# Kernel optimization log

Measured on AMD Instinct MI355X. Metric: run time of the kernel, lower is better.

Reference implementation:

```python
import jax, jax.numpy as jnp
import numpy as np

R_PARAM = 3.9
EPS = 0.3
BETA = 0.15
STEPS = 15
CLAMP_LO = 1e-4
CLAMP_HI = 1.0 - 1e-4


def _depthwise_conv3x3(x, k):
    # x: [B, C, H, W], k: [C, 1, 3, 3] (OIHW with feature_group_count=C)
    C = x.shape[1]
    return jax.lax.conv_general_dilated(
        x, k, window_strides=(1, 1), padding=((1, 1), (1, 1)),
        dimension_numbers=("NCHW", "OIHW", "NCHW"), feature_group_count=C)


def setup_inputs() -> dict:
    key = jax.random.key(0)
    k1, k2 = jax.random.split(key)
    drive = jax.random.uniform(k1, (16, 8, 256, 256), dtype=jnp.float32)
    K_raw = jnp.abs(jax.random.uniform(k2, (8, 1, 3, 3), dtype=jnp.float32))
    K_local = K_raw / K_raw.sum(axis=(-1, -2), keepdims=True)  # per-channel sum-to-1
    return {"drive": drive, "K_local": K_local}


def reference(drive, K_local):
    def step(grid, _):
        mapped = R_PARAM * grid * (1.0 - grid)
        local = _depthwise_conv3x3(mapped, K_local)
        physics = (1.0 - EPS) * mapped + EPS * local
        g = (1.0 - BETA) * physics + BETA * drive
        g = jnp.clip(g, CLAMP_LO, CLAMP_HI)
        return g, g

    last, states = jax.lax.scan(step, drive, None, length=STEPS)
    mean = states.mean(axis=0)
    var = ((states - mean) ** 2).mean(axis=0)  # unbiased=False
    delta = last - drive       # first == drive
    last_drive = last - drive
    return (last, mean, var, delta, last_drive)
```

## Files before the change

### kernel.cpp

```cpp
#include <hip/hip_runtime.h>
#include <cstddef>

namespace {

constexpr int IMG = 256;
constexpr long long N_ELEM = 16LL * 8 * IMG * IMG;

constexpr int NTHR   = 1024;
constexpr int DSTR   = 256;
constexpr int DSLOTS = 32;
constexpr int DBUF   = DSLOTS * DSTR;

constexpr float RP   = 3.9f;
constexpr float BET  = 0.15f;
constexpr float IBET = 1.0f / 0.15f;
constexpr float KF   = 0.255f;
constexpr float CF   = 0.595f;
constexpr float CLO  = 1e-4f;
constexpr float CHI  = (float)(1.0 - 1e-4);

__device__ __forceinline__ float mapf(float g) {
    float t = RP * g;
    return fmaf(-t, g, t);
}

__device__ __forceinline__ float dpp_up(float x) {
    return __int_as_float(__builtin_amdgcn_update_dpp(
        0, __float_as_int(x), 0x138, 0xf, 0xf, true));
}
__device__ __forceinline__ float dpp_dn(float x) {
    return __int_as_float(__builtin_amdgcn_update_dpp(
        0, __float_as_int(x), 0x130, 0xf, 0xf, true));
}

__device__ __forceinline__ float px9(const float k2[9],
        float a0, float a1, float a2, float b0, float b1, float b2,
        float c0, float c1, float c2, float bdv) {
    float a = bdv;
    a = fmaf(k2[0], a0, a); a = fmaf(k2[1], a1, a); a = fmaf(k2[2], a2, a);
    a = fmaf(k2[3], b0, a); a = fmaf(k2[4], b1, a); a = fmaf(k2[5], b2, a);
    a = fmaf(k2[6], c0, a); a = fmaf(k2[7], c1, a); a = fmaf(k2[8], c2, a);
    a = fmaf(CF, b1, a);
    return __builtin_amdgcn_fmed3f(a, CLO, CHI);
}

#define WINQ(W, QX, QY, QZ, QW) {                       \
    W[1] = (QX); W[2] = (QY); W[3] = (QZ); W[4] = (QW); \
    W[0] = dpp_up(QW);                                  \
    W[5] = dpp_dn(QX);                                  \
}

#define ROWB(WA, WB, WC, BDV, SUM, SQ, STG, OWN, F) {                                      \
    float g0 = px9(k2, WA[0],WA[1],WA[2], WB[0],WB[1],WB[2], WC[0],WC[1],WC[2], BDV.x);    \
    float g1 = px9(k2, WA[1],WA[2],WA[3], WB[1],WB[2],WB[3], WC[1],WC[2],WC[3], BDV.y);    \
    float g2 = px9(k2, WA[2],WA[3],WA[4], WB[2],WB[3],WB[4], WC[2],WC[3],WC[4], BDV.z);    \
    float g3 = px9(k2, WA[3],WA[4],WA[5], WB[3],WB[4],WB[5], WC[3],WC[4],WC[5], BDV.w);    \
    if (OWN) {                                                                             \
        SUM.x += g0; SUM.y += g1; SUM.z += g2; SUM.w += g3;                                \
        SQ.x = fmaf(g0,g0,SQ.x); SQ.y = fmaf(g1,g1,SQ.y);                                  \
        SQ.z = fmaf(g2,g2,SQ.z); SQ.w = fmaf(g3,g3,SQ.w);                                  \
    }                                                                                      \
    if (F) { STG.x = g0; STG.y = g1; STG.z = g2; STG.w = g3; }                             \
    else   { STG.x = mapf(g0); STG.y = mapf(g1); STG.z = mapf(g2); STG.w = mapf(g3); }     \
}

#define QLOAD(DR) \
    float4 qL, qR;                                                              \
    if (wv > 0)  qL = *(const float4*)((DR) + (2*wv - 1) * DSTR + c4);          \
    else { qL.x = 0.f; qL.y = 0.f; qL.z = 0.f; qL.w = 0.f; }                    \
    if (wv < 15) qR = *(const float4*)((DR) + (2*wv + 2) * DSTR + c4);          \
    else { qR.x = 0.f; qR.y = 0.f; qR.z = 0.f; qR.w = 0.f; }

#define STEP6(F, DR, DW) {                                                      \
    QLOAD(DR)                                                                   \
    float wA[6], wB[6], wC[6];                                                  \
    WINQ(wA, qL.x, qL.y, qL.z, qL.w)                                            \
    WINQ(wB, stg0.x, stg0.y, stg0.z, stg0.w)                                    \
    WINQ(wC, stg1.x, stg1.y, stg1.z, stg1.w)                                    \
    ROWB(wA, wB, wC, bdv0, sum0, sq0, stg0, ow0, F)                             \
    WINQ(wA, stg2.x, stg2.y, stg2.z, stg2.w)                                    \
    ROWB(wB, wC, wA, bdv1, sum1, sq1, stg1, ow1, F)                             \
    WINQ(wB, stg3.x, stg3.y, stg3.z, stg3.w)                                    \
    ROWB(wC, wA, wB, bdv2, sum2, sq2, stg2, ow2, F)                             \
    WINQ(wC, stg4.x, stg4.y, stg4.z, stg4.w)                                    \
    ROWB(wA, wB, wC, bdv3, sum3, sq3, stg3, ow3, F)                             \
    WINQ(wA, stg5.x, stg5.y, stg5.z, stg5.w)                                    \
    ROWB(wB, wC, wA, bdv4, sum4, sq4, stg4, ow4, F)                             \
    WINQ(wB, qR.x, qR.y, qR.z, qR.w)                                            \
    ROWB(wC, wA, wB, bdv5, sum5, sq5, stg5, ow5, F)                             \
    if (!(F)) {                                                                 \
        *(float4*)((DW) + (2*wv    ) * DSTR + c4) = stg0;                       \
        *(float4*)((DW) + (2*wv + 1) * DSTR + c4) = stg5;                       \
    }                                                                           \
}

#define STEP5(F, DR, DW) {                                                      \
    QLOAD(DR)                                                                   \
    float wA[6], wB[6], wC[6];                                                  \
    WINQ(wA, qL.x, qL.y, qL.z, qL.w)                                            \
    WINQ(wB, stg0.x, stg0.y, stg0.z, stg0.w)                                    \
    WINQ(wC, stg1.x, stg1.y, stg1.z, stg1.w)                                    \
    ROWB(wA, wB, wC, bdv0, sum0, sq0, stg0, ow0, F)                             \
    WINQ(wA, stg2.x, stg2.y, stg2.z, stg2.w)                                    \
    ROWB(wB, wC, wA, bdv1, sum1, sq1, stg1, ow1, F)                             \
    WINQ(wB, stg3.x, stg3.y, stg3.z, stg3.w)                                    \
    ROWB(wC, wA, wB, bdv2, sum2, sq2, stg2, ow2, F)                             \
    WINQ(wC, stg4.x, stg4.y, stg4.z, stg4.w)                                    \
    ROWB(wA, wB, wC, bdv3, sum3, sq3, stg3, ow3, F)                             \
    WINQ(wA, qR.x, qR.y, qR.z, qR.w)                                            \
    ROWB(wB, wC, wA, bdv4, sum4, sq4, stg4, ow4, F)                             \
    if (!(F)) {                                                                 \
        *(float4*)((DW) + (2*wv    ) * DSTR + c4) = stg0;                       \
        *(float4*)((DW) + (2*wv + 1) * DSTR + c4) = stg4;                       \
    }                                                                           \
}

#define INITROW(I, STRIDE) {                                                     \
    const int y = y0 + STRIDE * wv + (I);                                        \
    float4 t = *(const float4*)(dimg + y * IMG + c4);                            \
    stg##I.x = mapf(t.x); stg##I.y = mapf(t.y);                                  \
    stg##I.z = mapf(t.z); stg##I.w = mapf(t.w);                                  \
    bdv##I.x = BET * t.x; bdv##I.y = BET * t.y;                                  \
    bdv##I.z = BET * t.z; bdv##I.w = BET * t.w;                                  \
    sum##I.x = 0.f; sum##I.y = 0.f; sum##I.z = 0.f; sum##I.w = 0.f;              \
    sq##I = sum##I; }

#define EPISTORE(I) {                                                             \
    size_t base = (size_t)img * (IMG*IMG) + (size_t)y * IMG + c4;                 \
    float mn0 = sum##I.x*inv15, mn1 = sum##I.y*inv15;                             \
    float mn2 = sum##I.z*inv15, mn3 = sum##I.w*inv15;                             \
    float4 m4; m4.x=mn0; m4.y=mn1; m4.z=mn2; m4.w=mn3;                            \
    float4 v4;                                                                    \
    v4.x = fmaxf(fmaf(-mn0, mn0, sq##I.x*inv15), 0.f);                            \
    v4.y = fmaxf(fmaf(-mn1, mn1, sq##I.y*inv15), 0.f);                            \
    v4.z = fmaxf(fmaf(-mn2, mn2, sq##I.z*inv15), 0.f);                            \
    v4.w = fmaxf(fmaf(-mn3, mn3, sq##I.w*inv15), 0.f);                            \
    float4 d4;                                                                    \
    d4.x = fmaf(-bdv##I.x, IBET, stg##I.x); d4.y = fmaf(-bdv##I.y, IBET, stg##I.y);\
    d4.z = fmaf(-bdv##I.z, IBET, stg##I.z); d4.w = fmaf(-bdv##I.w, IBET, stg##I.w);\
    *(float4*)(out + 0*N_ELEM + base) = stg##I;                                   \
    *(float4*)(out + 1*N_ELEM + base) = m4;                                       \
    *(float4*)(out + 2*N_ELEM + base) = v4;                                       \
    *(float4*)(out + 3*N_ELEM + base) = d4;                                       \
    *(float4*)(out + 4*N_ELEM + base) = d4; }

__device__ __forceinline__ void run_int(const float* __restrict__ drive,
                                        const float* __restrict__ Kl,
                                        float* __restrict__ out,
                                        int img, int ty, float* __restrict__ lds)
{
    float* Da = lds;
    float* Db = lds + DBUF;
    const int tid  = threadIdx.x;
    const int lane = tid & 63;
    const int wv   = tid >> 6;
    const int c4   = lane * 4;

    const int lt = 6 * wv + 4;
    const int lb = 6 * (15 - wv) + 4;
    const int lim = min(15, min(lt, lb));

    const bool ow0 = (6*wv+0 >= 16) && (6*wv+0 <= 79);
    const bool ow1 = (6*wv+1 >= 16) && (6*wv+1 <= 79);
    const bool ow2 = (6*wv+2 >= 16) && (6*wv+2 <= 79);
    const bool ow3 = (6*wv+3 >= 16) && (6*wv+3 <= 79);
    const bool ow4 = (6*wv+4 >= 16) && (6*wv+4 <= 79);
    const bool ow5 = (6*wv+5 >= 16) && (6*wv+5 <= 79);

    const int ch = img & 7;
    float k2[9];
#pragma unroll
    for (int i = 0; i < 9; ++i) k2[i] = KF * Kl[ch * 9 + i];

    const float* dimg = drive + (size_t)img * (IMG * IMG);
    const int y0 = ty * 64 - 16;

    float4 bdv0,bdv1,bdv2,bdv3,bdv4,bdv5;
    float4 stg0,stg1,stg2,stg3,stg4,stg5;
    float4 sum0,sum1,sum2,sum3,sum4,sum5;
    float4 sq0,sq1,sq2,sq3,sq4,sq5;

    INITROW(0,6) INITROW(1,6) INITROW(2,6) INITROW(3,6) INITROW(4,6) INITROW(5,6)

    *(float4*)(Da + (2*wv    ) * DSTR + c4) = stg0;
    *(float4*)(Da + (2*wv + 1) * DSTR + c4) = stg5;
    __syncthreads();

#pragma unroll 1
    for (int s2 = 0; s2 < 7; ++s2) {
        if (2 * s2 < lim)     { STEP6(0, Da, Db) }
        __syncthreads();
        if (2 * s2 + 1 < lim) { STEP6(0, Db, Da) }
        __syncthreads();
    }
    if (lim >= 15) { STEP6(1, Da, Db) }

    if (wv >= 2 && wv <= 13) {
        const float inv15 = 1.0f / 15.0f;
#define EPI6(I) { const int r = 6*wv + (I);                                       \
        if (r >= 16 && r <= 79) { const int y = y0 + r; EPISTORE(I) } }
        EPI6(0) EPI6(1) EPI6(2) EPI6(3) EPI6(4) EPI6(5)
#undef EPI6
    }
}

template<bool TOP>
__device__ __forceinline__ void run_edge(const float* __restrict__ drive,
                                         const float* __restrict__ Kl,
                                         float* __restrict__ out,
                                         int img, float* __restrict__ lds)
{
    float* Da = lds;
    float* Db = lds + DBUF;
    const int tid  = threadIdx.x;
    const int lane = tid & 63;
    const int wv   = tid >> 6;
    const int c4   = lane * 4;

    const int lim = TOP ? min(15, 78 - 5 * wv) : min(15, 3 + 5 * wv);

    const bool ow0 = TOP ? (5*wv+0 <= 63) : (5*wv+0 >= 16);
    const bool ow1 = TOP ? (5*wv+1 <= 63) : (5*wv+1 >= 16);
    const bool ow2 = TOP ? (5*wv+2 <= 63) : (5*wv+2 >= 16);
    const bool ow3 = TOP ? (5*wv+3 <= 63) : (5*wv+3 >= 16);
    const bool ow4 = TOP ? (5*wv+4 <= 63) : (5*wv+4 >= 16);

    const int ch = img & 7;
    float k2[9];
#pragma unroll
    for (int i = 0; i < 9; ++i) k2[i] = KF * Kl[ch * 9 + i];

    const float* dimg = drive + (size_t)img * (IMG * IMG);
    const int y0 = TOP ? 0 : 176;

    float4 bdv0,bdv1,bdv2,bdv3,bdv4;
    float4 stg0,stg1,stg2,stg3,stg4;
    float4 sum0,sum1,sum2,sum3,sum4;
    float4 sq0,sq1,sq2,sq3,sq4;

    INITROW(0,5) INITROW(1,5) INITROW(2,5) INITROW(3,5) INITROW(4,5)

    *(float4*)(Da + (2*wv    ) * DSTR + c4) = stg0;
    *(float4*)(Da + (2*wv + 1) * DSTR + c4) = stg4;
    __syncthreads();

#pragma unroll 1
    for (int s2 = 0; s2 < 7; ++s2) {
        if (2 * s2 < lim)     { STEP5(0, Da, Db) }
        __syncthreads();
        if (2 * s2 + 1 < lim) { STEP5(0, Db, Da) }
        __syncthreads();
    }
    if (lim >= 15) { STEP5(1, Da, Db) }

    const bool own = TOP ? (wv <= 12) : (wv >= 3);
    if (own) {
        const float inv15 = 1.0f / 15.0f;
#define EPI5(I) { const int r = 5*wv + (I);                                       \
        if (TOP ? (r <= 63) : (r >= 16)) { const int y = y0 + r; EPISTORE(I) } }
        EPI5(0) EPI5(1) EPI5(2) EPI5(3) EPI5(4)
#undef EPI5
    }
}

__global__ __launch_bounds__(NTHR, 4)
void cml_kernel(const float* __restrict__ drive,
                const float* __restrict__ Kl,
                float* __restrict__ out)
{
    __shared__ __align__(16) float lds[2 * DBUF];
    const int bx  = blockIdx.x;
    const int img = bx >> 2;
    const int t   = bx & 3;
    if      (t == 0) run_edge<true >(drive, Kl, out, img, lds);
    else if (t == 3) run_edge<false>(drive, Kl, out, img, lds);
    else             run_int(drive, Kl, out, img, t, lds);
}

}

extern "C" void kernel_launch(void* const* d_in, const int* in_sizes, int n_in,
                              void* d_out, int out_size, void* d_ws, size_t ws_size,
                              hipStream_t stream) {
    const float* drive = (const float*)d_in[0];
    const float* Kl    = (const float*)d_in[1];
    float* out         = (float*)d_out;
    (void)in_sizes; (void)n_in; (void)out_size; (void)d_ws; (void)ws_size;

    dim3 grid(128 * 4);
    dim3 block(NTHR);
    cml_kernel<<<grid, block, 0, stream>>>(drive, Kl, out);
}
```

Measured before the change: 96.95 us.

## Replace block barriers with per-wave neighbor flag synchronization in LDS

The block-wide __syncthreads between stencil time steps is replaced by point-to-point sync. Each wave posts its step counter to a small LDS array and spins until its two adjacent waves have reached the same step before reading their halo rows. This lets waves drift relative to each other instead of all waiting on the slowest one every step. The cost is busy-wait spinning that takes issue slots, plus reliance on LDS fences and volatile polling being ordered correctly.

```diff
diff --git a/kernel.cpp b/kernel.cpp
--- a/kernel.cpp
+++ b/kernel.cpp
@@ -70,6 +70,16 @@
     else { qL.x = 0.f; qL.y = 0.f; qL.z = 0.f; qL.w = 0.f; }                    \
     if (wv < 15) qR = *(const float4*)((DR) + (2*wv + 2) * DSTR + c4);          \
     else { qR.x = 0.f; qR.y = 0.f; qR.z = 0.f; qR.w = 0.f; }
+
+#define SPIN(S) {                                                               \
+    if (wv > 0)  while (((volatile int*)cnt)[wv - 1] < (S)) {}                  \
+    if (wv < 15) while (((volatile int*)cnt)[wv + 1] < (S)) {}                  \
+    __threadfence_block();                                                      \
+}
+#define POST(S) {                                                               \
+    __threadfence_block();                                                      \
+    if (lane == 0) ((volatile int*)cnt)[wv] = (S);                              \
+}
 
 #define STEP6(F, DR, DW) {                                                      \
     QLOAD(DR)                                                                   \
@@ -147,7 +157,8 @@
 __device__ __forceinline__ void run_int(const float* __restrict__ drive,
                                         const float* __restrict__ Kl,
                                         float* __restrict__ out,
-                                        int img, int ty, float* __restrict__ lds)
+                                        int img, int ty, float* __restrict__ lds,
+                                        int* __restrict__ cnt)
 {
     float* Da = lds;
     float* Db = lds + DBUF;
@@ -182,18 +193,24 @@
 
     INITROW(0,6) INITROW(1,6) INITROW(2,6) INITROW(3,6) INITROW(4,6) INITROW(5,6)
 
+    if (tid < 16) cnt[tid] = 0;
     *(float4*)(Da + (2*wv    ) * DSTR + c4) = stg0;
     *(float4*)(Da + (2*wv + 1) * DSTR + c4) = stg5;
     __syncthreads();
 
+    const int limw = min(lim, 14);
+    int s = 0;
 #pragma unroll 1
-    for (int s2 = 0; s2 < 7; ++s2) {
-        if (2 * s2 < lim)     { STEP6(0, Da, Db) }
-        __syncthreads();
-        if (2 * s2 + 1 < lim) { STEP6(0, Db, Da) }
-        __syncthreads();
+    while (s < limw) {
+        const float* DR = (s & 1) ? Db : Da;
+        float*       DW = (s & 1) ? Da : Db;
+        SPIN(s)
+        STEP6(0, DR, DW)
+        POST(s + 1)
+        ++s;
     }
-    if (lim >= 15) { STEP6(1, Da, Db) }
+    if (lim >= 15) { SPIN(14) STEP6(1, Da, Db) }
+    else           { POST(99) }
 
     if (wv >= 2 && wv <= 13) {
         const float inv15 = 1.0f / 15.0f;
@@ -208,7 +225,8 @@
 __device__ __forceinline__ void run_edge(const float* __restrict__ drive,
                                          const float* __restrict__ Kl,
                                          float* __restrict__ out,
-                                         int img, float* __restrict__ lds)
+                                         int img, float* __restrict__ lds,
+                                         int* __restrict__ cnt)
 {
     float* Da = lds;
     float* Db = lds + DBUF;
@@ -240,18 +258,24 @@
 
     INITROW(0,5) INITROW(1,5) INITROW(2,5) INITROW(3,5) INITROW(4,5)
 
+    if (tid < 16) cnt[tid] = 0;
     *(float4*)(Da + (2*wv    ) * DSTR + c4) = stg0;
     *(float4*)(Da + (2*wv + 1) * DSTR + c4) = stg4;
     __syncthreads();
 
+    const int limw = min(lim, 14);
+    int s = 0;
 #pragma unroll 1
-    for (int s2 = 0; s2 < 7; ++s2) {
-        if (2 * s2 < lim)     { STEP5(0, Da, Db) }
-        __syncthreads();
-        if (2 * s2 + 1 < lim) { STEP5(0, Db, Da) }
-        __syncthreads();
+    while (s < limw) {
+        const float* DR = (s & 1) ? Db : Da;
+        float*       DW = (s & 1) ? Da : Db;
+        SPIN(s)
+        STEP5(0, DR, DW)
+        POST(s + 1)
+        ++s;
     }
-    if (lim >= 15) { STEP5(1, Da, Db) }
+    if (lim >= 15) { SPIN(14) STEP5(1, Da, Db) }
+    else           { POST(99) }
 
     const bool own = TOP ? (wv <= 12) : (wv >= 3);
     if (own) {
@@ -269,12 +293,13 @@
                 float* __restrict__ out)
 {
     __shared__ __align__(16) float lds[2 * DBUF];
+    __shared__ int cnt[16];
     const int bx  = blockIdx.x;
     const int img = bx >> 2;
     const int t   = bx & 3;
-    if      (t == 0) run_edge<true >(drive, Kl, out, img, lds);
-    else if (t == 3) run_edge<false>(drive, Kl, out, img, lds);
-    else             run_int(drive, Kl, out, img, t, lds);
+    if      (t == 0) run_edge<true >(drive, Kl, out, img, lds, cnt);
+    else if (t == 3) run_edge<false>(drive, Kl, out, img, lds, cnt);
+    else             run_int(drive, Kl, out, img, t, lds, cnt);
 }
 
 }
```

Result: slower. 105.0 us (+8.3%).
